# Kernel optimization log

Measured on AMD Instinct MI355X. Metric: run time of the kernel, lower is better.

The kernel has to match this reference:

```python
import jax, jax.numpy as jnp
import numpy as np

L, C, B = 256, 20, 1024


def _pos_mask(L):
    # pairwise mask: l2 - l1 >= 1, shape (L, L); broadcast over channels
    ls = jnp.arange(L)
    return (ls[None, :] - ls[:, None]) >= 1


def setup_inputs() -> dict:
    key = jax.random.key(0)
    k0, k1, k2 = jax.random.split(key, 3)
    x_lc = jax.random.uniform(k0, (B, L, C), dtype=jnp.float32)
    theta_0 = jnp.zeros((1,), dtype=jnp.float32)
    theta_lc = jax.random.normal(k1, (1, L, C), dtype=jnp.float32) / np.sqrt(L)
    pm = _pos_mask(L)
    theta_lclc = (jax.random.normal(k2, (1, L, C, L, C), dtype=jnp.float32)
                  / np.sqrt(L * L)) * pm[None, :, None, :, None]
    mask = pm
    return {"x_lc": x_lc, "theta_0": theta_0, "theta_lc": theta_lc,
            "theta_lclc": theta_lclc, "mask": mask}


def reference(x_lc, theta_0, theta_lc, theta_lclc, mask):
    Bn = x_lc.shape[0]
    # additive term: sum_{l,c} theta_lc * x
    phi = theta_0 + jnp.einsum('blc,zlc->b', x_lc, theta_lc)[:, None]
    # pairwise term as a masked bilinear form: x^T (mask * theta) x
    # (avoids materializing the (B,L,C,L,C) broadcast of the original)
    theta_m = theta_lclc[0] * mask[:, None, :, None].astype(theta_lclc.dtype)
    LC = L * C
    xf = x_lc.reshape(Bn, LC)                      # (B, LC)
    tf_ = theta_m.reshape(LC, LC)                  # (LC, LC)
    pair = jnp.einsum('bi,ij,bj->b', xf, tf_, xf)  # two GEMMs under the hood
    phi = phi + pair[:, None]
    return phi
```

## Files before the change

### kernel.cpp

```cpp
#include <hip/hip_runtime.h>
#include <stdint.h>

#define LDIM 256
#define CDIM 20
#define LC   5120
#define NB   1024
#define BM   128
#define BN   256
#define ITOT64 1640

typedef __attribute__((ext_vector_type(8))) short short8;
typedef __attribute__((ext_vector_type(4))) float float4v;
typedef __attribute__((ext_vector_type(4))) unsigned int uint4v;
typedef unsigned short ushort_t;

#define XB_BYTES (10485760ull)
#define WS_NEED  (XB_BYTES)

__device__ inline uint32_t pack_bf16x2(float a, float b) {
    uint32_t ua = __float_as_uint(a);
    uint32_t ub = __float_as_uint(b);
    ua += 0x7fffu + ((ua >> 16) & 1u);
    ub += 0x7fffu + ((ub >> 16) & 1u);
    return (ua >> 16) | (ub & 0xffff0000u);
}

__device__ inline float bf16_to_f32(ushort_t u) {
    return __uint_as_float(((uint32_t)u) << 16);
}

__device__ inline void load_lds16(const void* g, void* l) {
    __builtin_amdgcn_global_load_lds(
        (const __attribute__((address_space(1))) uint32_t*)g,
        (__attribute__((address_space(3))) uint32_t*)l, 16, 0, 0);
}

__global__ __launch_bounds__(256) void xconv_kernel(
    const float* __restrict__ X, const float* __restrict__ th0,
    const float* __restrict__ thlc, ushort_t* __restrict__ Xb,
    float* __restrict__ out)
{
    const int b = blockIdx.x;
    const int t = threadIdx.x;
    __shared__ float red[4];

    const float*  src = X  + (size_t)b * LC;
    ushort_t*     dst = Xb + (size_t)b * LC;
    float s = 0.f;
    for (int c = t * 4; c < LC; c += 1024) {
        float4 f = *(const float4*)(src + c);
        float4 w = *(const float4*)(thlc + c);
        s += f.x * w.x + f.y * w.y + f.z * w.z + f.w * w.w;
        uint2 u;
        u.x = pack_bf16x2(f.x, f.y);
        u.y = pack_bf16x2(f.z, f.w);
        *(uint2*)(dst + c) = u;
    }
    s += __shfl_xor(s, 1);  s += __shfl_xor(s, 2);  s += __shfl_xor(s, 4);
    s += __shfl_xor(s, 8);  s += __shfl_xor(s, 16); s += __shfl_xor(s, 32);
    if ((t & 63) == 0) red[t >> 6] = s;
    __syncthreads();
    if (t == 0) out[b] = th0[0] + red[0] + red[1] + red[2] + red[3];
}

__global__ __launch_bounds__(512, 2) void pair_fused(
    const float* __restrict__ T, const ushort_t* __restrict__ Xb,
    float* __restrict__ out)
{
    const int n    = blockIdx.x;
    const int bcol = (n >> 1) & 3;
    const int half = n & 1;
    const int kc   = n >> 3;
    const int bk64 = kc * 2 + half;
    const int bn0  = bcol * BN;

    const int gbeg = (ITOT64 * bk64) >> 6;
    const int gend = (ITOT64 * (bk64 + 1)) >> 6;

    int it = 0, pre = 0;
    while (pre + (80 - 2 * it) <= gbeg) { pre += 80 - 2 * it; ++it; }
    int li = gbeg - pre;

    __shared__ __align__(16) ushort_t A_s[1024 * 8];
    __shared__ __align__(16) ushort_t B_s[2][2048 * 8];

    const int t    = threadIdx.x;
    const int lane = t & 63;
    const int wid  = t >> 6;
    const int wm   = (wid >> 2) * 64;
    const int wn   = (wid & 3) * 64;
    const int l16  = lane & 15;
    const int qk   = lane >> 4;

    const int ga = t & 7;
    uint32_t offTa[2];
    int      wAdr[2];
    #pragma unroll
    for (int u = 0; u < 2; ++u) {
        const int row = (t >> 3) + u * 64;
        offTa[u] = (uint32_t)row * LC + (ga << 3);
        wAdr[u]  = ((row << 3) + (ga ^ (row & 7))) << 4;
    }

    uint32_t offB[4];
    int      ldsB[4];
    #pragma unroll
    for (int j = 0; j < 4; ++j) {
        const int c = (wid << 8) + (j << 6) + lane;
        const int row = c >> 3;
        const int g2 = (c & 7) ^ (row & 7);
        offB[j] = (uint32_t)(bn0 + row) * LC + (g2 << 3);
        ldsB[j] = ((wid << 8) + (j << 6)) << 3;
    }

    int adrA[2][4], adrB[2][4];
    #pragma unroll
    for (int step = 0; step < 2; ++step) {
        const int kf = step * 4 + qk;
        #pragma unroll
        for (int mt = 0; mt < 4; ++mt) {
            const int r = wm + mt * 16 + l16;
            adrA[step][mt] = ((r << 3) + (kf ^ (r & 7))) << 4;
        }
        #pragma unroll
        for (int nt = 0; nt < 4; ++nt) {
            const int r = wn + nt * 16 + l16;
            adrB[step][nt] = ((r << 3) + (kf ^ (r & 7))) << 4;
        }
    }

    int i0 = it << 7;
    int k0 = i0 + (li << 6);

    float4v acc[4][4];
    #pragma unroll
    for (int mt = 0; mt < 4; ++mt)
        #pragma unroll
        for (int nt = 0; nt < 4; ++nt)
            #pragma unroll
            for (int r = 0; r < 4; ++r) acc[mt][nt][r] = 0.f;

    float4 a0[2], a1[2];
    {
        const float* Tb0 = T + (size_t)i0 * LC + k0;
        #pragma unroll
        for (int u = 0; u < 2; ++u) {
            a0[u] = *(const float4*)(Tb0 + offTa[u]);
            a1[u] = *(const float4*)(Tb0 + offTa[u] + 4);
        }
        #pragma unroll
        for (int j = 0; j < 4; ++j)
            load_lds16(Xb + k0 + offB[j], &B_s[0][ldsB[j]]);
    }

    int cur = 0;

    for (int g = gbeg; g < gend; ++g) {
        const bool haveNext = (g + 1 < gend);
        const int  li_n   = li + 1;
        const bool segEnd = (li_n == 80 - 2 * it);
        const int  it_n   = segEnd ? it + 1 : it;
        const int  i0_n   = it_n << 7;
        const int  k0_n   = segEnd ? i0_n : (k0 + 64);

        __builtin_amdgcn_sched_barrier(0);
        __builtin_amdgcn_s_barrier();
        __builtin_amdgcn_sched_barrier(0);

        #pragma unroll
        for (int u = 0; u < 2; ++u) {
            uint4v v;
            v[0] = pack_bf16x2(a0[u].x, a0[u].y);
            v[1] = pack_bf16x2(a0[u].z, a0[u].w);
            v[2] = pack_bf16x2(a1[u].x, a1[u].y);
            v[3] = pack_bf16x2(a1[u].z, a1[u].w);
            *(uint4v*)((char*)A_s + wAdr[u]) = v;
        }

        if (haveNext) {
            const float* Tb2 = T + (size_t)i0_n * LC + k0_n;
            #pragma unroll
            for (int u = 0; u < 2; ++u) {
                a0[u] = *(const float4*)(Tb2 + offTa[u]);
                a1[u] = *(const float4*)(Tb2 + offTa[u] + 4);
            }
            #pragma unroll
            for (int j = 0; j < 4; ++j)
                load_lds16(Xb + k0_n + offB[j], &B_s[cur ^ 1][ldsB[j]]);
        }

        asm volatile("s_waitcnt lgkmcnt(0)" ::: "memory");
        __builtin_amdgcn_sched_barrier(0);
        if (haveNext)
            asm volatile("s_waitcnt vmcnt(8)" ::: "memory");
        else
            asm volatile("s_waitcnt vmcnt(0)" ::: "memory");
        __builtin_amdgcn_sched_barrier(0);
        __builtin_amdgcn_s_barrier();
        __builtin_amdgcn_sched_barrier(0);

        const char* Bbase = (const char*)B_s[cur];
        #pragma unroll
        for (int step = 0; step < 2; ++step) {
            short8 af[4], bfr[4];
            #pragma unroll
            for (int mt = 0; mt < 4; ++mt)
                af[mt] = *(const short8*)((const char*)A_s + adrA[step][mt]);
            #pragma unroll
            for (int nt = 0; nt < 4; ++nt)
                bfr[nt] = *(const short8*)(Bbase + adrB[step][nt]);
            __builtin_amdgcn_s_setprio(1);
            #pragma unroll
            for (int mt = 0; mt < 4; ++mt)
                #pragma unroll
                for (int nt = 0; nt < 4; ++nt)
                    acc[mt][nt] = __builtin_amdgcn_mfma_f32_16x16x32_bf16(
                        af[mt], bfr[nt], acc[mt][nt], 0, 0, 0);
            __builtin_amdgcn_s_setprio(0);
        }

        if (segEnd || !haveNext) {
            #pragma unroll
            for (int nt = 0; nt < 4; ++nt) {
                const int b = bn0 + wn + nt * 16 + l16;
                const ushort_t* xb = Xb + (size_t)b * LC + i0 + wm + qk * 4;
                float s = 0.f;
                #pragma unroll
                for (int mt = 0; mt < 4; ++mt) {
                    ushort4 xv = *(const ushort4*)(xb + mt * 16);
                    s += acc[mt][nt][0] * bf16_to_f32(xv.x)
                       + acc[mt][nt][1] * bf16_to_f32(xv.y)
                       + acc[mt][nt][2] * bf16_to_f32(xv.z)
                       + acc[mt][nt][3] * bf16_to_f32(xv.w);
                }
                s += __shfl_xor(s, 16);
                s += __shfl_xor(s, 32);
                if (qk == 0) atomicAdd(&out[b], s);
            }
            #pragma unroll
            for (int mt = 0; mt < 4; ++mt)
                #pragma unroll
                for (int nt = 0; nt < 4; ++nt)
                    #pragma unroll
                    for (int r = 0; r < 4; ++r) acc[mt][nt][r] = 0.f;
        }

        li = segEnd ? 0 : li_n;
        it = it_n;
        i0 = i0_n;
        k0 = k0_n;
        cur ^= 1;
    }
}

__global__ __launch_bounds__(256) void init_kernel(
    const float* __restrict__ x, const float* __restrict__ th0,
    const float* __restrict__ thlc, float* __restrict__ out)
{
    const int b = blockIdx.x;
    const float4* xb = (const float4*)(x + (size_t)b * LC);
    const float4* tv = (const float4*)thlc;
    float s = 0.f;
    for (int i = threadIdx.x; i < LC / 4; i += 256) {
        float4 a = xb[i], t = tv[i];
        s += a.x * t.x + a.y * t.y + a.z * t.z + a.w * t.w;
    }
    s += __shfl_xor(s, 1);  s += __shfl_xor(s, 2);  s += __shfl_xor(s, 4);
    s += __shfl_xor(s, 8);  s += __shfl_xor(s, 16); s += __shfl_xor(s, 32);
    __shared__ float red[4];
    if ((threadIdx.x & 63) == 0) red[threadIdx.x >> 6] = s;
    __syncthreads();
    if (threadIdx.x == 0) out[b] = th0[0] + red[0] + red[1] + red[2] + red[3];
}

__global__ __launch_bounds__(256) void pair_kernel(
    const float* __restrict__ T, const float* __restrict__ X,
    float* __restrict__ out)
{
    const int n  = blockIdx.x;
    const int r  = n & 7;
    const int g  = n >> 3;
    const int i0  = (g >> 3) * BM;
    const int bn0 = (g & 7) * 128;
    const int kstart = i0;
    const int nIter  = (LC - kstart) >> 6;
    const int ipc    = (nIter + 7) >> 3;
    const int itBeg  = r * ipc;
    const int itEnd  = (itBeg + ipc < nIter) ? (itBeg + ipc) : nIter;
    if (itBeg >= itEnd) return;
    const int kbeg   = kstart + (itBeg << 6);

    __shared__ __align__(16) short A_s[8 * BM * 8];
    __shared__ __align__(16) short B_s[8 * BM * 8];

    const int t    = threadIdx.x;
    const int lane = t & 63;
    const int wid  = t >> 6;
    const int wm   = (wid >> 1) * 64;
    const int wn   = (wid & 1) * 64;
    const int l16  = lane & 15;
    const int qk   = lane >> 4;

    const float* pA[4]; const float* pB[4]; int sIdx[4];
    #pragma unroll
    for (int u = 0; u < 4; ++u) {
        const int id  = t + u * 256;
        const int row = id >> 3;
        const int kq  = id & 7;
        pA[u] = T + (size_t)(i0 + row) * LC + kbeg + kq * 8;
        pB[u] = X + (size_t)(bn0 + row) * LC + kbeg + kq * 8;
        sIdx[u] = (kq * BM + (row ^ kq)) * 8;
    }

    float4v acc[4][4] = {};
    for (int itr = itBeg; itr < itEnd; ++itr) {
        __syncthreads();
        #pragma unroll
        for (int u = 0; u < 4; ++u) {
            float4 a0 = ((const float4*)pA[u])[0];
            float4 a1 = ((const float4*)pA[u])[1];
            float4 b0 = ((const float4*)pB[u])[0];
            float4 b1 = ((const float4*)pB[u])[1];
            pA[u] += 64; pB[u] += 64;
            uint4v va, vb;
            va[0] = pack_bf16x2(a0.x, a0.y); va[1] = pack_bf16x2(a0.z, a0.w);
            va[2] = pack_bf16x2(a1.x, a1.y); va[3] = pack_bf16x2(a1.z, a1.w);
            vb[0] = pack_bf16x2(b0.x, b0.y); vb[1] = pack_bf16x2(b0.z, b0.w);
            vb[2] = pack_bf16x2(b1.x, b1.y); vb[3] = pack_bf16x2(b1.z, b1.w);
            *(uint4v*)(A_s + sIdx[u]) = va;
            *(uint4v*)(B_s + sIdx[u]) = vb;
        }
        __syncthreads();
        #pragma unroll
        for (int step = 0; step < 2; ++step) {
            const int kf = step * 4 + qk;
            short8 af[4], bfr[4];
            #pragma unroll
            for (int mt = 0; mt < 4; ++mt)
                af[mt] = *(const short8*)(A_s + (kf * BM + ((wm + mt * 16 + l16) ^ kf)) * 8);
            #pragma unroll
            for (int nt = 0; nt < 4; ++nt)
                bfr[nt] = *(const short8*)(B_s + (kf * BM + ((wn + nt * 16 + l16) ^ kf)) * 8);
            #pragma unroll
            for (int mt = 0; mt < 4; ++mt)
                #pragma unroll
                for (int nt = 0; nt < 4; ++nt)
                    acc[mt][nt] = __builtin_amdgcn_mfma_f32_16x16x32_bf16(
                        af[mt], bfr[nt], acc[mt][nt], 0, 0, 0);
        }
    }
    #pragma unroll
    for (int nt = 0; nt < 4; ++nt) {
        const int b = bn0 + wn + nt * 16 + l16;
        const float* xb = X + (size_t)b * LC + i0 + wm + qk * 4;
        float s = 0.f;
        #pragma unroll
        for (int mt = 0; mt < 4; ++mt) {
            float4 xv = *(const float4*)(xb + mt * 16);
            s += acc[mt][nt][0] * xv.x + acc[mt][nt][1] * xv.y +
                 acc[mt][nt][2] * xv.z + acc[mt][nt][3] * xv.w;
        }
        s += __shfl_xor(s, 16);
        s += __shfl_xor(s, 32);
        if (qk == 0) atomicAdd(&out[b], s);
    }
}

extern "C" void kernel_launch(void* const* d_in, const int* in_sizes, int n_in,
                              void* d_out, int out_size, void* d_ws, size_t ws_size,
                              hipStream_t stream) {
    const float* x    = (const float*)d_in[0];
    const float* th0  = (const float*)d_in[1];
    const float* thlc = (const float*)d_in[2];
    const float* T    = (const float*)d_in[3];
    float* out = (float*)d_out;

    if (ws_size >= WS_NEED) {
        ushort_t* Xb = (ushort_t*)d_ws;
        xconv_kernel<<<NB, 256, 0, stream>>>(x, th0, thlc, Xb, out);
        pair_fused<<<256, 512, 0, stream>>>(T, Xb, out);
    } else {
        init_kernel<<<NB, 256, 0, stream>>>(x, th0, thlc, out);
        pair_kernel<<<(LC / BM) * (NB / 128) * 8, 256, 0, stream>>>(T, x, out);
    }
}
```

Baseline: 220.7 us.

## Shrink pair_fused tiles to 128x128 with 256 threads and quadruple grid

Changes the fused pair kernel from 512-thread blocks with a 128x256 output tile to 256-thread blocks with a 128x128 tile, splitting the batch columns into halves and the K range into twice as many chunks, for a 1024-block grid. Each block now loads four A rows per thread and uses smaller B buffers, and the LDS step addressing is recomputed with an XOR instead of a precomputed table, which frees registers. The goal is more blocks per CU and better load balance across the triangular K range. In exchange, the fp32 theta matrix is re-read by twice as many column tiles, raising global traffic, and atomic adds to the output increase.

```diff
diff --git a/kernel.cpp b/kernel.cpp
--- a/kernel.cpp
+++ b/kernel.cpp
@@ -6,7 +6,6 @@
 #define LC   5120
 #define NB   1024
 #define BM   128
-#define BN   256
 #define ITOT64 1640
 
 typedef __attribute__((ext_vector_type(8))) short short8;
@@ -63,70 +62,65 @@
     if (t == 0) out[b] = th0[0] + red[0] + red[1] + red[2] + red[3];
 }
 
-__global__ __launch_bounds__(512, 2) void pair_fused(
+__global__ __launch_bounds__(256, 3) void pair_fused(
     const float* __restrict__ T, const ushort_t* __restrict__ Xb,
     float* __restrict__ out)
 {
-    const int n    = blockIdx.x;
-    const int bcol = (n >> 1) & 3;
-    const int half = n & 1;
-    const int kc   = n >> 3;
-    const int bk64 = kc * 2 + half;
-    const int bn0  = bcol * BN;
-
-    const int gbeg = (ITOT64 * bk64) >> 6;
-    const int gend = (ITOT64 * (bk64 + 1)) >> 6;
+    const int n     = blockIdx.x;
+    const int khalf = n & 1;
+    const int bcol  = (n >> 1) & 3;
+    const int nhalf = (n >> 3) & 1;
+    const int kc    = n >> 4;
+    const int kblk  = kc * 2 + khalf;
+    const int bn0   = bcol * 256 + nhalf * 128;
+
+    const int gbeg = (ITOT64 * kblk) >> 7;
+    const int gend = (ITOT64 * (kblk + 1)) >> 7;
 
     int it = 0, pre = 0;
     while (pre + (80 - 2 * it) <= gbeg) { pre += 80 - 2 * it; ++it; }
     int li = gbeg - pre;
 
     __shared__ __align__(16) ushort_t A_s[1024 * 8];
-    __shared__ __align__(16) ushort_t B_s[2][2048 * 8];
+    __shared__ __align__(16) ushort_t B_s[2][1024 * 8];
 
     const int t    = threadIdx.x;
     const int lane = t & 63;
     const int wid  = t >> 6;
-    const int wm   = (wid >> 2) * 64;
-    const int wn   = (wid & 3) * 64;
+    const int wm   = (wid >> 1) * 64;
+    const int wn   = (wid & 1) * 64;
     const int l16  = lane & 15;
     const int qk   = lane >> 4;
 
     const int ga = t & 7;
-    uint32_t offTa[2];
-    int      wAdr[2];
-    #pragma unroll
-    for (int u = 0; u < 2; ++u) {
-        const int row = (t >> 3) + u * 64;
+    uint32_t offTa[4];
+    int      wAdr[4];
+    #pragma unroll
+    for (int u = 0; u < 4; ++u) {
+        const int row = u * 32 + (t >> 3);
         offTa[u] = (uint32_t)row * LC + (ga << 3);
         wAdr[u]  = ((row << 3) + (ga ^ (row & 7))) << 4;
     }
 
     uint32_t offB[4];
-    int      ldsB[4];
     #pragma unroll
     for (int j = 0; j < 4; ++j) {
         const int c = (wid << 8) + (j << 6) + lane;
         const int row = c >> 3;
         const int g2 = (c & 7) ^ (row & 7);
         offB[j] = (uint32_t)(bn0 + row) * LC + (g2 << 3);
-        ldsB[j] = ((wid << 8) + (j << 6)) << 3;
-    }
-
-    int adrA[2][4], adrB[2][4];
-    #pragma unroll
-    for (int step = 0; step < 2; ++step) {
-        const int kf = step * 4 + qk;
-        #pragma unroll
-        for (int mt = 0; mt < 4; ++mt) {
-            const int r = wm + mt * 16 + l16;
-            adrA[step][mt] = ((r << 3) + (kf ^ (r & 7))) << 4;
-        }
-        #pragma unroll
-        for (int nt = 0; nt < 4; ++nt) {
-            const int r = wn + nt * 16 + l16;
-            adrB[step][nt] = ((r << 3) + (kf ^ (r & 7))) << 4;
-        }
+    }
+
+    int adrA0[4], adrB0[4];
+    #pragma unroll
+    for (int mt = 0; mt < 4; ++mt) {
+        const int r = wm + mt * 16 + l16;
+        adrA0[mt] = ((r << 3) + (qk ^ (r & 7))) << 4;
+    }
+    #pragma unroll
+    for (int nt = 0; nt < 4; ++nt) {
+        const int r = wn + nt * 16 + l16;
+        adrB0[nt] = ((r << 3) + (qk ^ (r & 7))) << 4;
     }
 
     int i0 = it << 7;
@@ -140,17 +134,17 @@
             #pragma unroll
             for (int r = 0; r < 4; ++r) acc[mt][nt][r] = 0.f;
 
-    float4 a0[2], a1[2];
+    float4 a0[4], a1[4];
     {
         const float* Tb0 = T + (size_t)i0 * LC + k0;
         #pragma unroll
-        for (int u = 0; u < 2; ++u) {
+        for (int u = 0; u < 4; ++u) {
             a0[u] = *(const float4*)(Tb0 + offTa[u]);
             a1[u] = *(const float4*)(Tb0 + offTa[u] + 4);
         }
         #pragma unroll
         for (int j = 0; j < 4; ++j)
-            load_lds16(Xb + k0 + offB[j], &B_s[0][ldsB[j]]);
+            load_lds16(Xb + k0 + offB[j], &B_s[0][((wid << 8) + (j << 6)) << 3]);
     }
 
     int cur = 0;
@@ -168,7 +162,7 @@
         __builtin_amdgcn_sched_barrier(0);
 
         #pragma unroll
-        for (int u = 0; u < 2; ++u) {
+        for (int u = 0; u < 4; ++u) {
             uint4v v;
             v[0] = pack_bf16x2(a0[u].x, a0[u].y);
             v[1] = pack_bf16x2(a0[u].z, a0[u].w);
@@ -180,19 +174,20 @@
         if (haveNext) {
             const float* Tb2 = T + (size_t)i0_n * LC + k0_n;
             #pragma unroll
-            for (int u = 0; u < 2; ++u) {
+            for (int u = 0; u < 4; ++u) {
                 a0[u] = *(const float4*)(Tb2 + offTa[u]);
                 a1[u] = *(const float4*)(Tb2 + offTa[u] + 4);
             }
             #pragma unroll
             for (int j = 0; j < 4; ++j)
-                load_lds16(Xb + k0_n + offB[j], &B_s[cur ^ 1][ldsB[j]]);
+                load_lds16(Xb + k0_n + offB[j],
+                           &B_s[cur ^ 1][((wid << 8) + (j << 6)) << 3]);
         }
 
         asm volatile("s_waitcnt lgkmcnt(0)" ::: "memory");
         __builtin_amdgcn_sched_barrier(0);
         if (haveNext)
-            asm volatile("s_waitcnt vmcnt(8)" ::: "memory");
+            asm volatile("s_waitcnt vmcnt(12)" ::: "memory");
         else
             asm volatile("s_waitcnt vmcnt(0)" ::: "memory");
         __builtin_amdgcn_sched_barrier(0);
@@ -202,13 +197,14 @@
         const char* Bbase = (const char*)B_s[cur];
         #pragma unroll
         for (int step = 0; step < 2; ++step) {
+            const int sx = step << 6;
             short8 af[4], bfr[4];
             #pragma unroll
             for (int mt = 0; mt < 4; ++mt)
-                af[mt] = *(const short8*)((const char*)A_s + adrA[step][mt]);
+                af[mt] = *(const short8*)((const char*)A_s + (adrA0[mt] ^ sx));
             #pragma unroll
             for (int nt = 0; nt < 4; ++nt)
-                bfr[nt] = *(const short8*)(Bbase + adrB[step][nt]);
+                bfr[nt] = *(const short8*)(Bbase + (adrB0[nt] ^ sx));
             __builtin_amdgcn_s_setprio(1);
             #pragma unroll
             for (int mt = 0; mt < 4; ++mt)
@@ -378,7 +374,7 @@
     if (ws_size >= WS_NEED) {
         ushort_t* Xb = (ushort_t*)d_ws;
         xconv_kernel<<<NB, 256, 0, stream>>>(x, th0, thlc, Xb, out);
-        pair_fused<<<256, 512, 0, stream>>>(T, Xb, out);
+        pair_fused<<<1024, 256, 0, stream>>>(T, Xb, out);
     } else {
         init_kernel<<<NB, 256, 0, stream>>>(x, th0, thlc, out);
         pair_kernel<<<(LC / BM) * (NB / 128) * 8, 256, 0, stream>>>(T, x, out);
```

Result: no change. 217.4 us (-1.5%).
